# Kernel optimization log

Measured on AMD Instinct MI355X. Metric: run time of the kernel, lower is better.

The kernel has to match this reference:

```python
import jax, jax.numpy as jnp
import numpy as np

H = 8        # heads
W = 64       # window size
SHIFT = True
DIM = 512
SCALE = (DIM // H) ** -0.5


def setup_inputs() -> dict:
    key = jax.random.key(0)
    k1, k2, k3, k4 = jax.random.split(key, 4)
    x = jax.random.normal(k1, (8, 4096, DIM), dtype=jnp.float32)
    w_qkv = jax.random.normal(k2, (3 * DIM, DIM), dtype=jnp.float32) * 0.02
    w_proj = jax.random.normal(k3, (DIM, DIM), dtype=jnp.float32) * 0.02
    b_proj = jax.random.normal(k4, (DIM,), dtype=jnp.float32) * 0.02
    return {"x": x, "w_qkv": w_qkv, "w_proj": w_proj, "b_proj": b_proj}


def reference(x, w_qkv, w_proj, b_proj):
    B, N, C = x.shape
    if SHIFT:
        x = jnp.roll(x, -W // 2, axis=1)
    pad = (W - N % W) % W  # static Python int
    if pad:
        x = jnp.pad(x, ((0, 0), (0, pad), (0, 0)))
    nw = x.shape[1] // W
    xw = x.reshape(B * nw, W, C)                     # (B', W, C)
    qkv = xw @ w_qkv.T                               # (B', W, 3C)
    qkv = qkv.reshape(B * nw, W, 3, H, C // H)
    q, k, v = qkv[:, :, 0], qkv[:, :, 1], qkv[:, :, 2]  # (B', W, H, dh)
    # NOTE: faithful to source -- heads are NOT moved before matmul, so
    # attention is over the head axis: attn shape (B', W, H, H).
    attn = jnp.einsum('bwhd,bwgd->bwhg', q, k) * SCALE
    attn = jax.nn.softmax(attn, axis=-1)
    out = jnp.einsum('bwhg,bwgd->bwhd', attn, v)     # (B', W, H, dh)
    # transpose(1,2) then raw reshape, exactly as torch does (channel scramble)
    out = out.transpose(0, 2, 1, 3).reshape(B * nw, W, C)
    out = out @ w_proj.T + b_proj
    out = out.reshape(B, nw * W, C)[:, :N]
    if SHIFT:
        out = jnp.roll(out, W // 2, axis=1)
    return out
```

## Files before the change

### kernel.cpp

```cpp
#include <hip/hip_runtime.h>
#include <math.h>

typedef __attribute__((ext_vector_type(8))) short short8;
typedef __attribute__((ext_vector_type(4))) float float4v;

#define KDIM  512
#define NQKV  1536

__device__ __forceinline__ unsigned short f2bf(float f) {
    unsigned int u = __float_as_uint(f);
    u += 0x7FFFu + ((u >> 16) & 1u);
    return (unsigned short)(u >> 16);
}
__device__ __forceinline__ float bf2f(unsigned short u) {
    return __uint_as_float(((unsigned int)u) << 16);
}

__device__ __forceinline__ void gl2lds16(const unsigned short* g, unsigned short* l) {
    __builtin_amdgcn_global_load_lds(
        (const __attribute__((address_space(1))) void*)g,
        (__attribute__((address_space(3))) void*)l, 16, 0, 0);
}

__global__ __launch_bounds__(256) void cast_x_kernel(const float* __restrict__ x,
                                                     unsigned short* __restrict__ xb) {
    int tid = blockIdx.x * 256 + threadIdx.x;
    int t = tid >> 7;
    int c = (tid & 127) << 2;
    int b = t >> 12, n = t & 4095;
    int src = (b << 12) | ((n + 32) & 4095);
    float4 v = *(const float4*)(x + (((size_t)src) << 9) + c);
    ushort4 o;
    o.x = f2bf(v.x); o.y = f2bf(v.y); o.z = f2bf(v.z); o.w = f2bf(v.w);
    *(ushort4*)(xb + (((size_t)t) << 9) + c) = o;
}

__global__ __launch_bounds__(256) void cast_w_kernel(const float* __restrict__ wqkv,
                                                     const float* __restrict__ wproj,
                                                     unsigned short* __restrict__ wqkvb,
                                                     unsigned short* __restrict__ wprojb) {
    int tid = blockIdx.x * 256 + threadIdx.x;
    int e = tid << 2;
    if (e < NQKV * KDIM) {
        float4 v = *(const float4*)(wqkv + e);
        ushort4 o; o.x = f2bf(v.x); o.y = f2bf(v.y); o.z = f2bf(v.z); o.w = f2bf(v.w);
        *(ushort4*)(wqkvb + e) = o;
    } else {
        int e2 = e - NQKV * KDIM;
        float4 v = *(const float4*)(wproj + e2);
        ushort4 o; o.x = f2bf(v.x); o.y = f2bf(v.y); o.z = f2bf(v.z); o.w = f2bf(v.w);
        *(ushort4*)(wprojb + e2) = o;
    }
}

template<int N, bool PROJ>
__global__ __launch_bounds__(256, 2) void gemm_kernel(
        const unsigned short* __restrict__ A,
        const unsigned short* __restrict__ B,
        unsigned short* __restrict__ Cb,
        float* __restrict__ Cf,
        const float* __restrict__ bias) {
    __shared__ __align__(16) unsigned short As[128 * 64];
    __shared__ __align__(16) unsigned short Bs[128 * 64];
    const int bn = blockIdx.x, bm = blockIdx.y;
    const int tid = threadIdx.x;
    const int wave = tid >> 6, lane = tid & 63;
    const int quad = lane >> 4, l16 = lane & 15;
    const int wm = (wave >> 1) * 64, wn = (wave & 1) * 64;
    const int srow = lane >> 3;
    const int scol = ((lane & 7) ^ srow) * 8;

    float4v acc[4][4] = {};

    const unsigned short* Abase = A + (size_t)(bm * 128) * KDIM;
    const unsigned short* Bbase = B + (size_t)(bn * 128) * KDIM;

    for (int k0 = 0; k0 < KDIM; k0 += 64) {
        #pragma unroll
        for (int j = 0; j < 4; j++) {
            int chunk = j * 4 + wave;
            int row = chunk * 8 + srow;
            gl2lds16(Abase + (size_t)row * KDIM + k0 + scol, As + chunk * 512);
            gl2lds16(Bbase + (size_t)row * KDIM + k0 + scol, Bs + chunk * 512);
        }
        __syncthreads();
        #pragma unroll
        for (int ki = 0; ki < 2; ki++) {
            short8 af[4], bf[4];
            #pragma unroll
            for (int mi = 0; mi < 4; mi++) {
                int r = wm + mi * 16 + l16;
                int blk = (ki * 4 + quad) ^ (l16 & 7);
                af[mi] = *(const short8*)(As + r * 64 + blk * 8);
            }
            #pragma unroll
            for (int ni = 0; ni < 4; ni++) {
                int r = wn + ni * 16 + l16;
                int blk = (ki * 4 + quad) ^ (l16 & 7);
                bf[ni] = *(const short8*)(Bs + r * 64 + blk * 8);
            }
            #pragma unroll
            for (int mi = 0; mi < 4; mi++)
                #pragma unroll
                for (int ni = 0; ni < 4; ni++)
                    acc[mi][ni] = __builtin_amdgcn_mfma_f32_16x16x32_bf16(
                        af[mi], bf[ni], acc[mi][ni], 0, 0, 0);
        }
        __syncthreads();
    }

    #pragma unroll
    for (int mi = 0; mi < 4; mi++) {
        #pragma unroll
        for (int r = 0; r < 4; r++) {
            int m = bm * 128 + wm + mi * 16 + quad * 4 + r;
            if (!PROJ) {
                #pragma unroll
                for (int ni = 0; ni < 4; ni++) {
                    int n = bn * 128 + wn + ni * 16 + l16;
                    Cb[(size_t)m * N + n] = f2bf(acc[mi][ni][r]);
                }
            } else {
                int b = m >> 12, p = m & 4095;
                int nrow = (p + 32) & 4095;
                float* orow = Cf + (((size_t)((b << 12) | nrow)) << 9);
                #pragma unroll
                for (int ni = 0; ni < 4; ni++) {
                    int n = bn * 128 + wn + ni * 16 + l16;
                    orow[n] = acc[mi][ni][r] + bias[n];
                }
            }
        }
    }
}

#define TPB_TOK 16
#define KV_STRIDE 1032
__global__ __launch_bounds__(128) void attn_kernel(const unsigned short* __restrict__ qkvb,
                                                   unsigned short* __restrict__ aob) {
    __shared__ __align__(16) unsigned short smem[TPB_TOK * KV_STRIDE];
    const int tid = threadIdx.x;
    const int t0 = blockIdx.x * TPB_TOK;
    const int tok = tid >> 3, h = tid & 7;
    const int t = t0 + tok;

    short8 qs[8];
    {
        const unsigned short* qsrc = qkvb + (size_t)t * NQKV + h * 64;
        #pragma unroll
        for (int dc = 0; dc < 8; dc++)
            qs[dc] = *(const short8*)(qsrc + dc * 8);
    }

    {
        int r = tid >> 3, cb = (tid & 7) * 8;
        const unsigned short* src = qkvb + (size_t)(t0 + r) * NQKV + 512;
        unsigned short* dst = smem + r * KV_STRIDE;
        #pragma unroll
        for (int p = 0; p < 16; p++) {
            int c = cb + p * 64;
            *(short8*)(dst + c) = *(const short8*)(src + c);
        }
    }
    __syncthreads();

    const unsigned short* row = smem + tok * KV_STRIDE;

    float qv[64];
    #pragma unroll
    for (int dc = 0; dc < 8; dc++)
        #pragma unroll
        for (int j = 0; j < 8; j++)
            qv[dc * 8 + j] = bf2f((unsigned short)qs[dc][j]);

    float s[8];
    #pragma unroll
    for (int g = 0; g < 8; g++) {
        float acc = 0.f;
        #pragma unroll
        for (int dc = 0; dc < 8; dc++) {
            short8 ks = *(const short8*)(row + g * 64 + dc * 8);
            #pragma unroll
            for (int j = 0; j < 8; j++)
                acc += qv[dc * 8 + j] * bf2f((unsigned short)ks[j]);
        }
        s[g] = acc;
    }

    float mx = s[0];
    #pragma unroll
    for (int g = 1; g < 8; g++) mx = fmaxf(mx, s[g]);
    float p[8], sum = 0.f;
    #pragma unroll
    for (int g = 0; g < 8; g++) { p[g] = __expf((s[g] - mx) * 0.125f); sum += p[g]; }
    float inv = 1.f / sum;
    #pragma unroll
    for (int g = 0; g < 8; g++) p[g] *= inv;

    float o[64];
    #pragma unroll
    for (int j = 0; j < 64; j++) o[j] = 0.f;
    #pragma unroll
    for (int g = 0; g < 8; g++) {
        #pragma unroll
        for (int dc = 0; dc < 8; dc++) {
            short8 vs = *(const short8*)(row + 512 + g * 64 + dc * 8);
            #pragma unroll
            for (int j = 0; j < 8; j++)
                o[dc * 8 + j] += p[g] * bf2f((unsigned short)vs[j]);
        }
    }

    int win = t >> 6, w = t & 63;
    unsigned short* dst = aob + (size_t)(win * 64 + h * 8 + (w >> 3)) * 512 + (w & 7) * 64;
    #pragma unroll
    for (int dc = 0; dc < 16; dc++) {
        ushort4 ov;
        ov.x = f2bf(o[dc * 4 + 0]); ov.y = f2bf(o[dc * 4 + 1]);
        ov.z = f2bf(o[dc * 4 + 2]); ov.w = f2bf(o[dc * 4 + 3]);
        *(ushort4*)(dst + dc * 4) = ov;
    }
}

extern "C" void kernel_launch(void* const* d_in, const int* in_sizes, int n_in,
                              void* d_out, int out_size, void* d_ws, size_t ws_size,
                              hipStream_t stream) {
    const float* x      = (const float*)d_in[0];
    const float* w_qkv  = (const float*)d_in[1];
    const float* w_proj = (const float*)d_in[2];
    const float* b_proj = (const float*)d_in[3];
    float* out = (float*)d_out;

    char* ws = (char*)d_ws;
    unsigned short* xb     = (unsigned short*)(ws);
    unsigned short* wqkvb  = (unsigned short*)(ws + 33554432);
    unsigned short* wprojb = (unsigned short*)(ws + 35127296);
    unsigned short* qkvb   = (unsigned short*)(ws + 35651584);
    unsigned short* aob    = (unsigned short*)(ws + 136314880);

    cast_x_kernel<<<16384, 256, 0, stream>>>(x, xb);
    cast_w_kernel<<<1024, 256, 0, stream>>>(w_qkv, w_proj, wqkvb, wprojb);
    gemm_kernel<NQKV, false><<<dim3(12, 256), 256, 0, stream>>>(xb, wqkvb, qkvb, nullptr, nullptr);
    attn_kernel<<<2048, 128, 0, stream>>>(qkvb, aob);
    gemm_kernel<512, true><<<dim3(4, 256), 256, 0, stream>>>(aob, wprojb, nullptr, out, b_proj);
}
```

Baseline: 251.5 us.

## Double-buffer GEMM LDS loads with BK=32 and merge cast kernels into one launch

The GEMM main loop now uses two LDS buffers with a K-step of 32. The global-to-LDS DMA for step it+2 is issued while step it computes, synchronised by explicit vmcnt waits and raw barriers instead of two __syncthreads per step. This is meant to overlap memory latency with MFMA work. The swizzle pattern is reworked for the 32-wide rows. The two cast kernels are also merged into a single prep kernel to save one launch. The trade-offs are twice as many barrier rounds per K and correctness that depends on the hand-counted vmcnt values.

```diff
diff --git a/kernel.cpp b/kernel.cpp
--- a/kernel.cpp
+++ b/kernel.cpp
@@ -22,34 +22,36 @@
         (__attribute__((address_space(3))) void*)l, 16, 0, 0);
 }
 
-__global__ __launch_bounds__(256) void cast_x_kernel(const float* __restrict__ x,
-                                                     unsigned short* __restrict__ xb) {
-    int tid = blockIdx.x * 256 + threadIdx.x;
-    int t = tid >> 7;
-    int c = (tid & 127) << 2;
-    int b = t >> 12, n = t & 4095;
-    int src = (b << 12) | ((n + 32) & 4095);
-    float4 v = *(const float4*)(x + (((size_t)src) << 9) + c);
-    ushort4 o;
-    o.x = f2bf(v.x); o.y = f2bf(v.y); o.z = f2bf(v.z); o.w = f2bf(v.w);
-    *(ushort4*)(xb + (((size_t)t) << 9) + c) = o;
-}
-
-__global__ __launch_bounds__(256) void cast_w_kernel(const float* __restrict__ wqkv,
-                                                     const float* __restrict__ wproj,
-                                                     unsigned short* __restrict__ wqkvb,
-                                                     unsigned short* __restrict__ wprojb) {
-    int tid = blockIdx.x * 256 + threadIdx.x;
-    int e = tid << 2;
-    if (e < NQKV * KDIM) {
-        float4 v = *(const float4*)(wqkv + e);
-        ushort4 o; o.x = f2bf(v.x); o.y = f2bf(v.y); o.z = f2bf(v.z); o.w = f2bf(v.w);
-        *(ushort4*)(wqkvb + e) = o;
+__global__ __launch_bounds__(256) void prep_kernel(const float* __restrict__ x,
+                                                   const float* __restrict__ wqkv,
+                                                   const float* __restrict__ wproj,
+                                                   unsigned short* __restrict__ xb,
+                                                   unsigned short* __restrict__ wqkvb,
+                                                   unsigned short* __restrict__ wprojb) {
+    int bid = blockIdx.x;
+    if (bid < 16384) {
+        int tid = bid * 256 + threadIdx.x;
+        int t = tid >> 7;
+        int c = (tid & 127) << 2;
+        int b = t >> 12, n = t & 4095;
+        int src = (b << 12) | ((n + 32) & 4095);
+        float4 v = *(const float4*)(x + (((size_t)src) << 9) + c);
+        ushort4 o;
+        o.x = f2bf(v.x); o.y = f2bf(v.y); o.z = f2bf(v.z); o.w = f2bf(v.w);
+        *(ushort4*)(xb + (((size_t)t) << 9) + c) = o;
     } else {
-        int e2 = e - NQKV * KDIM;
-        float4 v = *(const float4*)(wproj + e2);
-        ushort4 o; o.x = f2bf(v.x); o.y = f2bf(v.y); o.z = f2bf(v.z); o.w = f2bf(v.w);
-        *(ushort4*)(wprojb + e2) = o;
+        int tid = (bid - 16384) * 256 + threadIdx.x;
+        int e = tid << 2;
+        if (e < NQKV * KDIM) {
+            float4 v = *(const float4*)(wqkv + e);
+            ushort4 o; o.x = f2bf(v.x); o.y = f2bf(v.y); o.z = f2bf(v.z); o.w = f2bf(v.w);
+            *(ushort4*)(wqkvb + e) = o;
+        } else {
+            int e2 = e - NQKV * KDIM;
+            float4 v = *(const float4*)(wproj + e2);
+            ushort4 o; o.x = f2bf(v.x); o.y = f2bf(v.y); o.z = f2bf(v.z); o.w = f2bf(v.w);
+            *(ushort4*)(wprojb + e2) = o;
+        }
     }
 }
 
@@ -60,53 +62,61 @@
         unsigned short* __restrict__ Cb,
         float* __restrict__ Cf,
         const float* __restrict__ bias) {
-    __shared__ __align__(16) unsigned short As[128 * 64];
-    __shared__ __align__(16) unsigned short Bs[128 * 64];
+    __shared__ __align__(16) unsigned short As[2][4096];
+    __shared__ __align__(16) unsigned short Bs[2][4096];
     const int bn = blockIdx.x, bm = blockIdx.y;
     const int tid = threadIdx.x;
     const int wave = tid >> 6, lane = tid & 63;
     const int quad = lane >> 4, l16 = lane & 15;
     const int wm = (wave >> 1) * 64, wn = (wave & 1) * 64;
-    const int srow = lane >> 3;
-    const int scol = ((lane & 7) ^ srow) * 8;
+    const int srow = lane >> 2;
+    const int scol = ((lane & 3) ^ ((srow >> 1) & 3)) * 8;
 
     float4v acc[4][4] = {};
 
     const unsigned short* Abase = A + (size_t)(bm * 128) * KDIM;
     const unsigned short* Bbase = B + (size_t)(bn * 128) * KDIM;
 
-    for (int k0 = 0; k0 < KDIM; k0 += 64) {
-        #pragma unroll
-        for (int j = 0; j < 4; j++) {
+    auto dma = [&](int k0, int buf) {
+        #pragma unroll
+        for (int j = 0; j < 2; j++) {
             int chunk = j * 4 + wave;
-            int row = chunk * 8 + srow;
-            gl2lds16(Abase + (size_t)row * KDIM + k0 + scol, As + chunk * 512);
-            gl2lds16(Bbase + (size_t)row * KDIM + k0 + scol, Bs + chunk * 512);
-        }
-        __syncthreads();
-        #pragma unroll
-        for (int ki = 0; ki < 2; ki++) {
-            short8 af[4], bf[4];
+            int row = chunk * 16 + srow;
+            gl2lds16(Abase + (size_t)row * KDIM + k0 + scol, &As[buf][chunk * 512]);
+            gl2lds16(Bbase + (size_t)row * KDIM + k0 + scol, &Bs[buf][chunk * 512]);
+        }
+    };
+
+    dma(0, 0);
+    dma(32, 1);
+
+    const int rblk = ((l16 >> 1) & 3);
+
+    #pragma unroll
+    for (int it = 0; it < 16; ++it) {
+        if (it < 15) asm volatile("s_waitcnt vmcnt(4)" ::: "memory");
+        else         asm volatile("s_waitcnt vmcnt(0)" ::: "memory");
+        asm volatile("s_barrier" ::: "memory");
+        const int buf = it & 1;
+        short8 af[4], bf[4];
+        #pragma unroll
+        for (int mi = 0; mi < 4; mi++) {
+            int r = wm + mi * 16 + l16;
+            af[mi] = *(const short8*)(&As[buf][r * 32 + ((quad ^ rblk) * 8)]);
+        }
+        #pragma unroll
+        for (int ni = 0; ni < 4; ni++) {
+            int r = wn + ni * 16 + l16;
+            bf[ni] = *(const short8*)(&Bs[buf][r * 32 + ((quad ^ rblk) * 8)]);
+        }
+        #pragma unroll
+        for (int mi = 0; mi < 4; mi++)
             #pragma unroll
-            for (int mi = 0; mi < 4; mi++) {
-                int r = wm + mi * 16 + l16;
-                int blk = (ki * 4 + quad) ^ (l16 & 7);
-                af[mi] = *(const short8*)(As + r * 64 + blk * 8);
-            }
-            #pragma unroll
-            for (int ni = 0; ni < 4; ni++) {
-                int r = wn + ni * 16 + l16;
-                int blk = (ki * 4 + quad) ^ (l16 & 7);
-                bf[ni] = *(const short8*)(Bs + r * 64 + blk * 8);
-            }
-            #pragma unroll
-            for (int mi = 0; mi < 4; mi++)
-                #pragma unroll
-                for (int ni = 0; ni < 4; ni++)
-                    acc[mi][ni] = __builtin_amdgcn_mfma_f32_16x16x32_bf16(
-                        af[mi], bf[ni], acc[mi][ni], 0, 0, 0);
-        }
-        __syncthreads();
+            for (int ni = 0; ni < 4; ni++)
+                acc[mi][ni] = __builtin_amdgcn_mfma_f32_16x16x32_bf16(
+                    af[mi], bf[ni], acc[mi][ni], 0, 0, 0);
+        asm volatile("s_barrier" ::: "memory");
+        if (it < 14) dma((it + 2) * 32, buf);
     }
 
     #pragma unroll
@@ -238,8 +248,7 @@
     unsigned short* qkvb   = (unsigned short*)(ws + 35651584);
     unsigned short* aob    = (unsigned short*)(ws + 136314880);
 
-    cast_x_kernel<<<16384, 256, 0, stream>>>(x, xb);
-    cast_w_kernel<<<1024, 256, 0, stream>>>(w_qkv, w_proj, wqkvb, wprojb);
+    prep_kernel<<<16384 + 1024, 256, 0, stream>>>(x, w_qkv, w_proj, xb, wqkvb, wprojb);
     gemm_kernel<NQKV, false><<<dim3(12, 256), 256, 0, stream>>>(xb, wqkvb, qkvb, nullptr, nullptr);
     attn_kernel<<<2048, 128, 0, stream>>>(qkvb, aob);
     gemm_kernel<512, true><<<dim3(4, 256), 256, 0, stream>>>(aob, wprojb, nullptr, out, b_proj);
```

New measurement: 261.0 us. +3.8%, slower.
